# Performance work log

Measured on AMD Instinct MI355X. Metric: run time of the kernel, lower is better.

## Reference

```python
import jax, jax.numpy as jnp
import numpy as np

N_NODES, N_EDGES = 50000, 800000
IN_X, OUT_X = 32, 64
IN_EN, OUT_EN = 32, 64
HIDDEN = [64, 128, 32]  # build_mlp hidden sizes


def _mlp_params(key, dims):
    ps = []
    for i, (a, b) in enumerate(zip(dims[:-1], dims[1:])):
        k1, k2, key = jax.random.split(key, 3)
        s = 1.0 / np.sqrt(a)
        ps.append(jax.random.uniform(k1, (a, b), jnp.float32, -s, s))
        ps.append(jax.random.uniform(k2, (b,), jnp.float32, -s, s))
    return ps


def _mlp_apply(h, params):
    n_layers = len(params) // 2
    for i in range(n_layers):
        W, b = params[2 * i], params[2 * i + 1]
        h = h @ W + b
        if i < n_layers - 1:
            h = jax.nn.relu(h)
    return h


def setup_inputs() -> dict:
    key = jax.random.key(0)
    kx, ken, ks, kd, kt, kp, k_ten, k_pen = jax.random.split(key, 8)
    inp = {
        "x": jax.random.normal(kx, (N_NODES, IN_X), jnp.float32),
        "en": jax.random.normal(ken, (N_NODES, IN_EN), jnp.float32),
        "src": jax.random.randint(ks, (N_EDGES,), 0, N_NODES),
        "dst": jax.random.randint(kd, (N_EDGES,), 0, N_NODES),
    }
    # linear layers theta/phi for x
    kt1, kt2 = jax.random.split(kt)
    kp1, kp2 = jax.random.split(kp)
    s = 1.0 / np.sqrt(IN_X)
    inp["theta_W"] = jax.random.uniform(kt1, (IN_X, OUT_X), jnp.float32, -s, s)
    inp["theta_b"] = jax.random.uniform(kt2, (OUT_X,), jnp.float32, -s, s)
    inp["phi_W"] = jax.random.uniform(kp1, (IN_X, OUT_X), jnp.float32, -s, s)
    inp["phi_b"] = jax.random.uniform(kp2, (OUT_X,), jnp.float32, -s, s)
    # MLPs theta_en / phi_en: in_en -> 64 -> 128 -> 32 -> out_en
    dims = [IN_EN] + HIDDEN + [OUT_EN]
    for name, p in zip(
        ["ten_W0", "ten_b0", "ten_W1", "ten_b1", "ten_W2", "ten_b2", "ten_W3", "ten_b3"],
        _mlp_params(k_ten, dims)):
        inp[name] = p
    for name, p in zip(
        ["pen_W0", "pen_b0", "pen_W1", "pen_b1", "pen_W2", "pen_b2", "pen_W3", "pen_b3"],
        _mlp_params(k_pen, dims)):
        inp[name] = p
    return inp


def reference(x, en, src, dst,
              theta_W, theta_b, phi_W, phi_b,
              ten_W0, ten_b0, ten_W1, ten_b1, ten_W2, ten_b2, ten_W3, ten_b3,
              pen_W0, pen_b0, pen_W1, pen_b1, pen_W2, pen_b2, pen_W3, pen_b3):
    n = x.shape[0]
    ten = [ten_W0, ten_b0, ten_W1, ten_b1, ten_W2, ten_b2, ten_W3, ten_b3]
    pen = [pen_W0, pen_b0, pen_W1, pen_b1, pen_W2, pen_b2, pen_W3, pen_b3]

    # --- message: per-edge features ---
    dx = x[dst] - x[src]                       # [E, in_x]
    edge_x = dx @ theta_W + theta_b + (x @ phi_W + phi_b)[src]   # [E, out_x]
    den = en[dst] - en[src]                    # [E, in_en]
    edge_en = _mlp_apply(den, ten) + _mlp_apply(en, pen)[src]    # [E, out_en]

    # --- aggregate: max over incoming edge_x, mean over incoming edge_en ---
    deg = jax.ops.segment_sum(jnp.ones((src.shape[0],), x.dtype), dst, num_segments=n)
    has_in = (deg > 0)[:, None]
    x_new = jax.ops.segment_max(edge_x, dst, num_segments=n)
    x_new = jnp.where(has_in, x_new, 0.0)      # DGL zero-fills empty nodes
    en_sum = jax.ops.segment_sum(edge_en, dst, num_segments=n)
    en_new = en_sum / jnp.maximum(deg, 1.0)[:, None]

    # knn_graph rebuild is a library call (excluded from the kernel target);
    # return the updated node features carried by the new graph.
    return jnp.concatenate([x_new, en_new], axis=-1)  # [N, out_x + out_en]
```

## Files before the change

### kernel.cpp

```cpp
#include <hip/hip_runtime.h>

#define N_NODES 50000
#define N_EDGES 800000

typedef __attribute__((ext_vector_type(8))) short short8v;
typedef __attribute__((ext_vector_type(4))) float f32x4;

constexpr int M_W0T = 0;
constexpr int M_B0  = 2048;
constexpr int M_W1T = 2112;
constexpr int M_B1  = 10304;
constexpr int M_W2  = 10432;
constexpr int M_B2  = 14528;
constexpr int M_SZ  = 14560;

__device__ __forceinline__ void stage_mlp(float* sm,
    const float* __restrict__ W0, const float* __restrict__ b0,
    const float* __restrict__ W1, const float* __restrict__ b1,
    const float* __restrict__ W2, const float* __restrict__ b2,
    int tid, int nthr) {
  for (int t = tid; t < 2048; t += nthr) {
    int j = t >> 5, k = t & 31;
    sm[M_W0T + t] = W0[k * 64 + j];
  }
  for (int t = tid; t < 8192; t += nthr) {
    int k2 = t >> 6, j = t & 63;
    sm[M_W1T + t] = W1[j * 128 + k2];
  }
  for (int t = tid; t < 4096; t += nthr) sm[M_W2 + t] = W2[t];
  for (int t = tid; t < 64; t += nthr)  sm[M_B0 + t] = b0[t];
  for (int t = tid; t < 128; t += nthr) sm[M_B1 + t] = b1[t];
  for (int t = tid; t < 32; t += nthr)  sm[M_B2 + t] = b2[t];
}

__device__ __forceinline__ void mlp_core(const float* sm, const float den[32],
                                         float h2[32]) {
  float h0[64];
#pragma unroll
  for (int j = 0; j < 64; ++j) {
    float a = sm[M_B0 + j];
#pragma unroll
    for (int k = 0; k < 32; ++k) a += den[k] * sm[M_W0T + j * 32 + k];
    h0[j] = fmaxf(a, 0.f);
  }
#pragma unroll
  for (int j = 0; j < 32; ++j) h2[j] = sm[M_B2 + j];
  for (int k2 = 0; k2 < 128; ++k2) {
    float t = sm[M_B1 + k2];
#pragma unroll
    for (int j = 0; j < 64; ++j) t += h0[j] * sm[M_W1T + k2 * 64 + j];
    t = fmaxf(t, 0.f);
#pragma unroll
    for (int j = 0; j < 32; ++j) h2[j] += t * sm[M_W2 + k2 * 32 + j];
  }
#pragma unroll
  for (int j = 0; j < 32; ++j) h2[j] = fmaxf(h2[j], 0.f);
}

__device__ __forceinline__ ushort bf16hi(float v) {
  return (ushort)(__float_as_uint(v) >> 16);
}

constexpr int EK_TW0 = 0;
constexpr int EK_MLP = 2048;
constexpr int EK_W3T = 16608;
constexpr int EK_B3  = 18656;
constexpr int EK_SZ  = 18720;

#define CA_EN 196
#define CA_CNT 3125
#define CA_PACK 48

__global__ void __launch_bounds__(256) combo_a_kernel(
    const float* __restrict__ en, const float* __restrict__ tW0,
    const float* __restrict__ pW0, const float* __restrict__ pb0,
    const float* __restrict__ pW1, const float* __restrict__ pb1,
    const float* __restrict__ pW2, const float* __restrict__ pb2,
    const float* __restrict__ pW3, const float* __restrict__ pb3,
    float* __restrict__ gp, float* __restrict__ u,
    const int* __restrict__ dst, int* __restrict__ counts,
    const float* __restrict__ tW1, const float* __restrict__ tW2,
    ushort* __restrict__ wp) {
  const int b = blockIdx.x;
  const int tid = threadIdx.x;
  if (b < CA_EN) {
    __shared__ __align__(16) float sm[EK_SZ];
    for (int t = tid; t < 2048; t += 256) {
      int j = t >> 5, k = t & 31;
      sm[EK_TW0 + t] = tW0[k * 64 + j];
      sm[EK_W3T + t] = pW3[k * 64 + j];
    }
    for (int t = tid; t < 64; t += 256) sm[EK_B3 + t] = pb3[t];
    stage_mlp(sm + EK_MLP, pW0, pb0, pW1, pb1, pW2, pb2, tid, 256);
    __syncthreads();
    int n = b * 256 + tid;
    if (n >= N_NODES) return;

    float ev[32];
    {
      const float4* p = (const float4*)(en + (long)n * 32);
#pragma unroll
      for (int q = 0; q < 8; ++q) {
        float4 v = p[q];
        ev[q * 4 + 0] = v.x; ev[q * 4 + 1] = v.y;
        ev[q * 4 + 2] = v.z; ev[q * 4 + 3] = v.w;
      }
    }
    float* uo = u + (long)n * 64;
    for (int j = 0; j < 64; ++j) {
      float a = 0.f;
#pragma unroll
      for (int k = 0; k < 32; ++k) a += ev[k] * sm[EK_TW0 + j * 32 + k];
      uo[j] = a;
    }
    float h2p[32];
    mlp_core(sm + EK_MLP, ev, h2p);
    float* go = gp + (long)n * 128 + 64;
    for (int j = 0; j < 64; ++j) {
      float o = sm[EK_B3 + j];
#pragma unroll
      for (int k = 0; k < 32; ++k) o += h2p[k] * sm[EK_W3T + j * 32 + k];
      go[j] = o;
    }
  } else if (b < CA_EN + CA_CNT) {
    int e = (b - CA_EN) * 256 + tid;
    if (e < N_EDGES) atomicAdd(&counts[dst[e]], 1);
  } else {
    int t = (b - CA_EN - CA_CNT) * 256 + tid;
    if (t >= 12288) return;
    float v;
    int hi_off, lo_off;
    if (t < 8192) {
      int fi = t >> 9, lane = (t >> 3) & 63, j = t & 7;
      int r = fi >> 1, f = fi & 1;
      int k2 = r * 16 + (lane & 15);
      int jg = f * 32 + (lane >> 4) * 8 + j;
      v = tW1[jg * 128 + k2];
      hi_off = t; lo_off = 8192 + t;
    } else {
      int t2 = t - 8192;
      int fi = t2 >> 9, lane = (t2 >> 3) & 63, j = t2 & 7;
      int tt = fi >> 2, f2 = fi & 3;
      int cc = tt * 16 + (lane & 15);
      int q = (lane >> 4) & 3;
      int k2 = f2 * 32 + (j >> 2) * 16 + q * 4 + (j & 3);
      v = tW2[k2 * 32 + cc];
      hi_off = 16384 + t2; lo_off = 20480 + t2;
    }
    ushort h = bf16hi(v);
    float hf = __uint_as_float((unsigned)h << 16);
    ushort l = bf16hi(v - hf);
    wp[hi_off] = h;
    wp[lo_off] = l;
  }
}

#define SCAN_NB ((N_NODES + 1023) / 1024)

__global__ void __launch_bounds__(1024) scan1_kernel(
    const int* __restrict__ counts, int* __restrict__ offsets,
    int* __restrict__ bsum) {
  __shared__ int wsum[16];
  int t = threadIdx.x, b = blockIdx.x;
  int idx = b * 1024 + t;
  int c = (idx < N_NODES) ? counts[idx] : 0;
  int lane = t & 63, w = t >> 6;
  int v = c;
#pragma unroll
  for (int off = 1; off < 64; off <<= 1) {
    int tt = __shfl_up(v, off);
    if (lane >= off) v += tt;
  }
  if (lane == 63) wsum[w] = v;
  __syncthreads();
  int wpre = 0;
#pragma unroll
  for (int i = 0; i < 16; ++i) {
    int tt = wsum[i];
    if (i < w) wpre += tt;
  }
  int incl = v + wpre;
  if (idx < N_NODES) offsets[idx] = incl - c;
  if (t == 1023) bsum[b] = incl;
}

__global__ void __launch_bounds__(1024) scan2_kernel(
    const int* __restrict__ bsum, int* __restrict__ offsets,
    int* __restrict__ counts) {
  __shared__ int sb[SCAN_NB];
  int t = threadIdx.x, b = blockIdx.x;
  if (t < SCAN_NB) sb[t] = bsum[t];
  __syncthreads();
  int bpre = 0;
#pragma unroll
  for (int i = 0; i < SCAN_NB; ++i) {
    int tt = sb[i];
    if (i < b) bpre += tt;
  }
  int idx = b * 1024 + t;
  if (idx < N_NODES) {
    int v = offsets[idx] + bpre;
    offsets[idx] = v;
    counts[idx] = v;
  }
  if (b == 0 && t == 0) offsets[N_NODES] = N_EDGES;
}

#define CB_X 196
#define CB_SC 3125

constexpr int XK_THT = 0;
constexpr int XK_PHT = 2048;
constexpr int XK_THB = 4096;
constexpr int XK_PHB = 4160;
constexpr int XK_SZ  = 4224;

__global__ void __launch_bounds__(256) combo_b_kernel(
    const float* __restrict__ x,
    const float* __restrict__ thW, const float* __restrict__ thB,
    const float* __restrict__ phW, const float* __restrict__ phB,
    float* __restrict__ out, float* __restrict__ gp,
    const int* __restrict__ src, const int* __restrict__ dst,
    int* __restrict__ cursor, int2* __restrict__ csr) {
  const int b = blockIdx.x;
  const int tid = threadIdx.x;
  if (b < CB_X) {
    __shared__ __align__(16) float sm[XK_SZ];
    for (int t = tid; t < 2048; t += 256) {
      int j = t >> 5, k = t & 31;
      sm[XK_THT + t] = thW[k * 64 + j];
      sm[XK_PHT + t] = phW[k * 64 + j];
    }
    for (int t = tid; t < 64; t += 256) {
      sm[XK_THB + t] = thB[t];
      sm[XK_PHB + t] = phB[t];
    }
    __syncthreads();
    int n = b * 256 + tid;
    if (n >= N_NODES) return;

    float xv[32];
    {
      const float4* p = (const float4*)(x + (long)n * 32);
#pragma unroll
      for (int q = 0; q < 8; ++q) {
        float4 v = p[q];
        xv[q * 4 + 0] = v.x; xv[q * 4 + 1] = v.y;
        xv[q * 4 + 2] = v.z; xv[q * 4 + 3] = v.w;
      }
    }
    float* ao = out + (long)n * 128;
    float* go = gp + (long)n * 128;
    for (int j = 0; j < 64; ++j) {
      float dth = 0.f, dph = 0.f;
#pragma unroll
      for (int k = 0; k < 32; ++k) {
        dth += xv[k] * sm[XK_THT + j * 32 + k];
        dph += xv[k] * sm[XK_PHT + j * 32 + k];
      }
      ao[j] = sm[XK_THB + j] + dth;
      go[j] = sm[XK_PHB + j] + dph - dth;
    }
  } else {
    int e = (b - CB_X) * 256 + tid;
    if (e >= N_EDGES) return;
    int d = dst[e];
    int slot = atomicAdd(&cursor[d], 1);
    csr[slot] = make_int2(src[e], d);
  }
}

__global__ void __launch_bounds__(512) mlp_edge_kernel(
    const float* __restrict__ u,
    const int2* __restrict__ csr,
    const float* __restrict__ b0g, const float* __restrict__ b1g,
    const float* __restrict__ b2g,
    const ushort* __restrict__ wp,
    float* __restrict__ h2sum) {
  __shared__ __align__(16) ushort lds[24576];
  {
    const uint4* s4 = (const uint4*)wp;
    uint4* d4 = (uint4*)lds;
    for (int i = threadIdx.x; i < 3072; i += 512) d4[i] = s4[i];
  }
  __syncthreads();

  const int orig = blockIdx.x;
  const int xcd = orig & 7, loc = orig >> 3;
  const int blk = (xcd < 2) ? xcd * 782 + loc
                            : 2 * 782 + (xcd - 2) * 781 + loc;

  const int lane = threadIdx.x & 63;
  const int q = lane >> 4, c = lane & 15;
  const int wv = threadIdx.x >> 6;
  const int e = (blk * 8 + wv) * 16 + c;
  const int2 pr = csr[e];
  const int s = pr.x, d = pr.y;

  const short8v* W1HI = (const short8v*)(lds);
  const short8v* W1LO = (const short8v*)(lds + 8192);
  const short8v* W2HI = (const short8v*)(lds + 16384);
  const short8v* W2LO = (const short8v*)(lds + 20480);

  short8v bh0, bl0, bh1, bl1;
  {
    const float* ud = u + (long)d * 64 + q * 8;
    const float* us = u + (long)s * 64 + q * 8;
    const float* bp = b0g + q * 8;
#pragma unroll
    for (int f = 0; f < 2; ++f) {
      float4 d0 = *(const float4*)(ud + f * 32);
      float4 d1 = *(const float4*)(ud + f * 32 + 4);
      float4 s0 = *(const float4*)(us + f * 32);
      float4 s1 = *(const float4*)(us + f * 32 + 4);
      float4 c0 = *(const float4*)(bp + f * 32);
      float4 c1 = *(const float4*)(bp + f * 32 + 4);
      float v[8];
      v[0] = fmaxf(d0.x - s0.x + c0.x, 0.f);
      v[1] = fmaxf(d0.y - s0.y + c0.y, 0.f);
      v[2] = fmaxf(d0.z - s0.z + c0.z, 0.f);
      v[3] = fmaxf(d0.w - s0.w + c0.w, 0.f);
      v[4] = fmaxf(d1.x - s1.x + c1.x, 0.f);
      v[5] = fmaxf(d1.y - s1.y + c1.y, 0.f);
      v[6] = fmaxf(d1.z - s1.z + c1.z, 0.f);
      v[7] = fmaxf(d1.w - s1.w + c1.w, 0.f);
      short8v hh, ll;
#pragma unroll
      for (int j = 0; j < 8; ++j) {
        unsigned uv = __float_as_uint(v[j]);
        hh[j] = (short)(uv >> 16);
        float hf = __uint_as_float(uv & 0xFFFF0000u);
        ll[j] = (short)(__float_as_uint(v[j] - hf) >> 16);
      }
      if (f == 0) { bh0 = hh; bl0 = ll; } else { bh1 = hh; bl1 = ll; }
    }
  }

  f32x4 acc[8];
#pragma unroll
  for (int r = 0; r < 8; ++r)
    acc[r] = *(const f32x4*)(b1g + r * 16 + q * 4);
#pragma unroll
  for (int r = 0; r < 8; ++r) {
    short8v ah0 = W1HI[(2 * r) * 64 + lane];
    short8v ah1 = W1HI[(2 * r + 1) * 64 + lane];
    short8v al0 = W1LO[(2 * r) * 64 + lane];
    short8v al1 = W1LO[(2 * r + 1) * 64 + lane];
    acc[r] = __builtin_amdgcn_mfma_f32_16x16x32_bf16(ah0, bh0, acc[r], 0, 0, 0);
    acc[r] = __builtin_amdgcn_mfma_f32_16x16x32_bf16(ah1, bh1, acc[r], 0, 0, 0);
    acc[r] = __builtin_amdgcn_mfma_f32_16x16x32_bf16(al0, bh0, acc[r], 0, 0, 0);
    acc[r] = __builtin_amdgcn_mfma_f32_16x16x32_bf16(al1, bh1, acc[r], 0, 0, 0);
    acc[r] = __builtin_amdgcn_mfma_f32_16x16x32_bf16(ah0, bl0, acc[r], 0, 0, 0);
    acc[r] = __builtin_amdgcn_mfma_f32_16x16x32_bf16(ah1, bl1, acc[r], 0, 0, 0);
  }
  float h1v[8][4];
#pragma unroll
  for (int r = 0; r < 8; ++r)
#pragma unroll
    for (int g = 0; g < 4; ++g) h1v[r][g] = fmaxf(acc[r][g], 0.f);

  short8v b2h[4], b2l[4];
#pragma unroll
  for (int f2 = 0; f2 < 4; ++f2) {
    short8v hh, ll;
#pragma unroll
    for (int j = 0; j < 8; ++j) {
      float v = h1v[2 * f2 + (j >> 2)][j & 3];
      unsigned uv = __float_as_uint(v);
      hh[j] = (short)(uv >> 16);
      float hf = __uint_as_float(uv & 0xFFFF0000u);
      ll[j] = (short)(__float_as_uint(v - hf) >> 16);
    }
    b2h[f2] = hh; b2l[f2] = ll;
  }

  f32x4 a20 = *(const f32x4*)(b2g + q * 4);
  f32x4 a21 = *(const f32x4*)(b2g + 16 + q * 4);
#pragma unroll
  for (int f2 = 0; f2 < 4; ++f2) {
    short8v ah = W2HI[f2 * 64 + lane];
    short8v al = W2LO[f2 * 64 + lane];
    a20 = __builtin_amdgcn_mfma_f32_16x16x32_bf16(ah, b2h[f2], a20, 0, 0, 0);
    a20 = __builtin_amdgcn_mfma_f32_16x16x32_bf16(al, b2h[f2], a20, 0, 0, 0);
    a20 = __builtin_amdgcn_mfma_f32_16x16x32_bf16(ah, b2l[f2], a20, 0, 0, 0);
    short8v ah1 = W2HI[(4 + f2) * 64 + lane];
    short8v al1 = W2LO[(4 + f2) * 64 + lane];
    a21 = __builtin_amdgcn_mfma_f32_16x16x32_bf16(ah1, b2h[f2], a21, 0, 0, 0);
    a21 = __builtin_amdgcn_mfma_f32_16x16x32_bf16(al1, b2h[f2], a21, 0, 0, 0);
    a21 = __builtin_amdgcn_mfma_f32_16x16x32_bf16(ah1, b2l[f2], a21, 0, 0, 0);
  }
  float h2v[8];
#pragma unroll
  for (int g = 0; g < 4; ++g) {
    h2v[g] = fmaxf(a20[g], 0.f);
    h2v[4 + g] = fmaxf(a21[g], 0.f);
  }

  int dp = __shfl_up(d, 1, 16);
  bool head = (c == 0) || (dp != d);
  int seg = head ? c : 0;
#pragma unroll
  for (int off = 1; off < 16; off <<= 1) {
    int t = __shfl_up(seg, off, 16);
    if (c >= off) seg = max(seg, t);
  }
#pragma unroll
  for (int off = 1; off < 16; off <<= 1) {
    bool take = (c - off) >= seg;
#pragma unroll
    for (int k = 0; k < 8; ++k) {
      float t = __shfl_up(h2v[k], off, 16);
      if (take) h2v[k] += t;
    }
  }
  int dn = __shfl_down(d, 1, 16);
  bool tail = (c == 15) || (dn != d);
  if (tail) {
    float* hs = h2sum + (long)d * 32 + q * 4;
#pragma unroll
    for (int g = 0; g < 4; ++g) atomicAdd(&hs[g], h2v[g]);
#pragma unroll
    for (int g = 0; g < 4; ++g) atomicAdd(&hs[16 + g], h2v[4 + g]);
  }
}

__global__ void __launch_bounds__(256) gather_kernel(
    const int2* __restrict__ csr, const int* __restrict__ offsets,
    const float* __restrict__ gp, const float* __restrict__ h2sum,
    const float* __restrict__ tW3, const float* __restrict__ tb3,
    float* __restrict__ out) {
  __shared__ float sW3[2048 + 64];
  for (int t = threadIdx.x; t < 2048; t += 256) sW3[t] = tW3[t];
  for (int t = threadIdx.x; t < 64; t += 256) sW3[2048 + t] = tb3[t];
  __syncthreads();
  int n = blockIdx.x * 8 + (threadIdx.x >> 5);
  int l = threadIdx.x & 31;
  int half = l >> 4, j4 = l & 15;
  int off = half * 64 + j4 * 4;
  int o0 = offsets[n], o1 = offsets[n + 1];
  int deg = o1 - o0;

  const float NEG = -3.402823466e38f;
  float4 mx = make_float4(NEG, NEG, NEG, NEG);
  float4 sm4 = make_float4(0.f, 0.f, 0.f, 0.f);
  for (int t = o0; t < o1; ++t) {
    int s = csr[t].x;
    float4 v = *(const float4*)(gp + (long)s * 128 + off);
    mx.x = fmaxf(mx.x, v.x); mx.y = fmaxf(mx.y, v.y);
    mx.z = fmaxf(mx.z, v.z); mx.w = fmaxf(mx.w, v.w);
    sm4.x += v.x; sm4.y += v.y; sm4.z += v.z; sm4.w += v.w;
  }

  float4 r;
  if (half == 0) {
    float4 a = *(const float4*)(out + (long)n * 128 + off);
    bool has = deg > 0;
    r.x = has ? a.x + mx.x : 0.f;
    r.y = has ? a.y + mx.y : 0.f;
    r.z = has ? a.z + mx.z : 0.f;
    r.w = has ? a.w + mx.w : 0.f;
  } else {
    int jj = j4 * 4;
    float w30 = 0.f, w31 = 0.f, w32 = 0.f, w33 = 0.f;
    const float* h2r = h2sum + (long)n * 32;
#pragma unroll
    for (int k = 0; k < 32; ++k) {
      float h = h2r[k];
      const float* wrow = &sW3[k * 64 + jj];
      w30 += h * wrow[0]; w31 += h * wrow[1];
      w32 += h * wrow[2]; w33 += h * wrow[3];
    }
    float dg = (float)deg;
    float inv = 1.f / fmaxf(dg, 1.f);
    r.x = (sm4.x + w30 + dg * sW3[2048 + jj + 0]) * inv;
    r.y = (sm4.y + w31 + dg * sW3[2048 + jj + 1]) * inv;
    r.z = (sm4.z + w32 + dg * sW3[2048 + jj + 2]) * inv;
    r.w = (sm4.w + w33 + dg * sW3[2048 + jj + 3]) * inv;
  }
  *(float4*)(out + (long)n * 128 + off) = r;
}

extern "C" void kernel_launch(void* const* d_in, const int* in_sizes, int n_in,
                              void* d_out, int out_size, void* d_ws,
                              size_t ws_size, hipStream_t stream) {
  const float* x   = (const float*)d_in[0];
  const float* en  = (const float*)d_in[1];
  const int* src   = (const int*)d_in[2];
  const int* dst   = (const int*)d_in[3];
  const float* thW = (const float*)d_in[4];
  const float* thB = (const float*)d_in[5];
  const float* phW = (const float*)d_in[6];
  const float* phB = (const float*)d_in[7];
  const float* tW0 = (const float*)d_in[8];
  const float* tb0 = (const float*)d_in[9];
  const float* tW1 = (const float*)d_in[10];
  const float* tb1 = (const float*)d_in[11];
  const float* tW2 = (const float*)d_in[12];
  const float* tb2 = (const float*)d_in[13];
  const float* tW3 = (const float*)d_in[14];
  const float* tb3 = (const float*)d_in[15];
  const float* pW0 = (const float*)d_in[16];
  const float* pb0 = (const float*)d_in[17];
  const float* pW1 = (const float*)d_in[18];
  const float* pb1 = (const float*)d_in[19];
  const float* pW2 = (const float*)d_in[20];
  const float* pb2 = (const float*)d_in[21];
  const float* pW3 = (const float*)d_in[22];
  const float* pb3 = (const float*)d_in[23];

  float* out = (float*)d_out;
  float* ws  = (float*)d_ws;
  float* gp     = ws;
  float* u      = ws + (long)N_NODES * 128;
  float* h2sum  = ws + (long)N_NODES * 192;
  float* wpf    = ws + (long)N_NODES * 224;
  ushort* wp    = (ushort*)wpf;
  int* iw       = (int*)(wpf + 12288);
  int2* csr     = (int2*)iw;
  int* counts   = iw + 2 * N_EDGES;
  int* offsets  = counts + N_NODES;
  int* bsum     = offsets + N_NODES + 1;

  hipMemsetAsync(counts, 0, N_NODES * sizeof(int), stream);
  hipMemsetAsync(h2sum, 0, (size_t)N_NODES * 32 * sizeof(float), stream);
  combo_a_kernel<<<CA_EN + CA_CNT + CA_PACK, 256, 0, stream>>>(
      en, tW0, pW0, pb0, pW1, pb1, pW2, pb2, pW3, pb3, gp, u,
      dst, counts, tW1, tW2, wp);
  scan1_kernel<<<SCAN_NB, 1024, 0, stream>>>(counts, offsets, bsum);
  scan2_kernel<<<SCAN_NB, 1024, 0, stream>>>(bsum, offsets, counts);
  combo_b_kernel<<<CB_X + CB_SC, 256, 0, stream>>>(
      x, thW, thB, phW, phB, out, gp, src, dst, counts, csr);
  mlp_edge_kernel<<<N_EDGES / 128, 512, 0, stream>>>(
      u, csr, tb0, tb1, tb2, wp, h2sum);
  gather_kernel<<<N_NODES / 8, 256, 0, stream>>>(
      csr, offsets, gp, h2sum, tW3, tb3, out);
}
```

Baseline: 355.2 us.

## Move per-node phi_en MLP and theta_en projection onto split-bf16 MFMA

The per-node MLP (phi_en) and the node-level theta_en first-layer projection previously ran as scalar FP32 loops from LDS, one thread per node. They now run on 16x16x32 bf16 MFMA with a hi/lo split of the weights, prepacked into a shared buffer. The x-linear work moves into the first combo kernel, and the node MLP joins the CSR scatter kernel, so the MLP can consume the packed weights. This aims to cut the ALU-bound per-node MLP cost, at the price of a larger packing stage, 72KB of LDS per block, and three-product split-bf16 accuracy instead of full FP32.

```diff
diff --git a/kernel.cpp b/kernel.cpp
--- a/kernel.cpp
+++ b/kernel.cpp
@@ -6,128 +6,85 @@
 typedef __attribute__((ext_vector_type(8))) short short8v;
 typedef __attribute__((ext_vector_type(4))) float f32x4;
 
-constexpr int M_W0T = 0;
-constexpr int M_B0  = 2048;
-constexpr int M_W1T = 2112;
-constexpr int M_B1  = 10304;
-constexpr int M_W2  = 10432;
-constexpr int M_B2  = 14528;
-constexpr int M_SZ  = 14560;
-
-__device__ __forceinline__ void stage_mlp(float* sm,
-    const float* __restrict__ W0, const float* __restrict__ b0,
-    const float* __restrict__ W1, const float* __restrict__ b1,
-    const float* __restrict__ W2, const float* __restrict__ b2,
-    int tid, int nthr) {
-  for (int t = tid; t < 2048; t += nthr) {
-    int j = t >> 5, k = t & 31;
-    sm[M_W0T + t] = W0[k * 64 + j];
-  }
-  for (int t = tid; t < 8192; t += nthr) {
-    int k2 = t >> 6, j = t & 63;
-    sm[M_W1T + t] = W1[j * 128 + k2];
-  }
-  for (int t = tid; t < 4096; t += nthr) sm[M_W2 + t] = W2[t];
-  for (int t = tid; t < 64; t += nthr)  sm[M_B0 + t] = b0[t];
-  for (int t = tid; t < 128; t += nthr) sm[M_B1 + t] = b1[t];
-  for (int t = tid; t < 32; t += nthr)  sm[M_B2 + t] = b2[t];
-}
-
-__device__ __forceinline__ void mlp_core(const float* sm, const float den[32],
-                                         float h2[32]) {
-  float h0[64];
-#pragma unroll
-  for (int j = 0; j < 64; ++j) {
-    float a = sm[M_B0 + j];
-#pragma unroll
-    for (int k = 0; k < 32; ++k) a += den[k] * sm[M_W0T + j * 32 + k];
-    h0[j] = fmaxf(a, 0.f);
-  }
-#pragma unroll
-  for (int j = 0; j < 32; ++j) h2[j] = sm[M_B2 + j];
-  for (int k2 = 0; k2 < 128; ++k2) {
-    float t = sm[M_B1 + k2];
-#pragma unroll
-    for (int j = 0; j < 64; ++j) t += h0[j] * sm[M_W1T + k2 * 64 + j];
-    t = fmaxf(t, 0.f);
-#pragma unroll
-    for (int j = 0; j < 32; ++j) h2[j] += t * sm[M_W2 + k2 * 32 + j];
-  }
-#pragma unroll
-  for (int j = 0; j < 32; ++j) h2[j] = fmaxf(h2[j], 0.f);
-}
-
 __device__ __forceinline__ ushort bf16hi(float v) {
   return (ushort)(__float_as_uint(v) >> 16);
 }
 
-constexpr int EK_TW0 = 0;
-constexpr int EK_MLP = 2048;
-constexpr int EK_W3T = 16608;
-constexpr int EK_B3  = 18656;
-constexpr int EK_SZ  = 18720;
-
-#define CA_EN 196
-#define CA_CNT 3125
-#define CA_PACK 48
-
-__global__ void __launch_bounds__(256) combo_a_kernel(
-    const float* __restrict__ en, const float* __restrict__ tW0,
-    const float* __restrict__ pW0, const float* __restrict__ pb0,
-    const float* __restrict__ pW1, const float* __restrict__ pb1,
-    const float* __restrict__ pW2, const float* __restrict__ pb2,
-    const float* __restrict__ pW3, const float* __restrict__ pb3,
-    float* __restrict__ gp, float* __restrict__ u,
+__device__ __forceinline__ void split8(const float v[8], short8v& hh, short8v& ll) {
+#pragma unroll
+  for (int j = 0; j < 8; ++j) {
+    unsigned uv = __float_as_uint(v[j]);
+    hh[j] = (short)(uv >> 16);
+    float hf = __uint_as_float(uv & 0xFFFF0000u);
+    ll[j] = (short)(__float_as_uint(v[j] - hf) >> 16);
+  }
+}
+
+#define C1_X 196
+#define C1_CNT 3125
+#define C1_PACK 120
+
+constexpr int XK_THT = 0;
+constexpr int XK_PHT = 2048;
+constexpr int XK_THB = 4096;
+constexpr int XK_PHB = 4160;
+constexpr int XK_SZ  = 4224;
+
+__global__ void __launch_bounds__(256) combo1_kernel(
+    const float* __restrict__ x,
+    const float* __restrict__ thW, const float* __restrict__ thB,
+    const float* __restrict__ phW, const float* __restrict__ phB,
+    float* __restrict__ out, float* __restrict__ gp,
     const int* __restrict__ dst, int* __restrict__ counts,
     const float* __restrict__ tW1, const float* __restrict__ tW2,
-    ushort* __restrict__ wp) {
+    const float* __restrict__ tW0, const float* __restrict__ pW0,
+    const float* __restrict__ pW1, const float* __restrict__ pW2,
+    const float* __restrict__ pW3, ushort* __restrict__ wp) {
   const int b = blockIdx.x;
   const int tid = threadIdx.x;
-  if (b < CA_EN) {
-    __shared__ __align__(16) float sm[EK_SZ];
+  if (b < C1_X) {
+    __shared__ __align__(16) float sm[XK_SZ];
     for (int t = tid; t < 2048; t += 256) {
       int j = t >> 5, k = t & 31;
-      sm[EK_TW0 + t] = tW0[k * 64 + j];
-      sm[EK_W3T + t] = pW3[k * 64 + j];
-    }
-    for (int t = tid; t < 64; t += 256) sm[EK_B3 + t] = pb3[t];
-    stage_mlp(sm + EK_MLP, pW0, pb0, pW1, pb1, pW2, pb2, tid, 256);
+      sm[XK_THT + t] = thW[k * 64 + j];
+      sm[XK_PHT + t] = phW[k * 64 + j];
+    }
+    for (int t = tid; t < 64; t += 256) {
+      sm[XK_THB + t] = thB[t];
+      sm[XK_PHB + t] = phB[t];
+    }
     __syncthreads();
     int n = b * 256 + tid;
     if (n >= N_NODES) return;
 
-    float ev[32];
+    float xv[32];
     {
-      const float4* p = (const float4*)(en + (long)n * 32);
+      const float4* p = (const float4*)(x + (long)n * 32);
 #pragma unroll
       for (int q = 0; q < 8; ++q) {
         float4 v = p[q];
-        ev[q * 4 + 0] = v.x; ev[q * 4 + 1] = v.y;
-        ev[q * 4 + 2] = v.z; ev[q * 4 + 3] = v.w;
+        xv[q * 4 + 0] = v.x; xv[q * 4 + 1] = v.y;
+        xv[q * 4 + 2] = v.z; xv[q * 4 + 3] = v.w;
       }
     }
-    float* uo = u + (long)n * 64;
+    float* ao = out + (long)n * 128;
+    float* go = gp + (long)n * 128;
     for (int j = 0; j < 64; ++j) {
-      float a = 0.f;
-#pragma unroll
-      for (int k = 0; k < 32; ++k) a += ev[k] * sm[EK_TW0 + j * 32 + k];
-      uo[j] = a;
-    }
-    float h2p[32];
-    mlp_core(sm + EK_MLP, ev, h2p);
-    float* go = gp + (long)n * 128 + 64;
-    for (int j = 0; j < 64; ++j) {
-      float o = sm[EK_B3 + j];
-#pragma unroll
-      for (int k = 0; k < 32; ++k) o += h2p[k] * sm[EK_W3T + j * 32 + k];
-      go[j] = o;
-    }
-  } else if (b < CA_EN + CA_CNT) {
-    int e = (b - CA_EN) * 256 + tid;
+      float dth = 0.f, dph = 0.f;
+#pragma unroll
+      for (int k = 0; k < 32; ++k) {
+        dth += xv[k] * sm[XK_THT + j * 32 + k];
+        dph += xv[k] * sm[XK_PHT + j * 32 + k];
+      }
+      ao[j] = sm[XK_THB + j] + dth;
+      go[j] = sm[XK_PHB + j] + dph - dth;
+    }
+  } else if (b < C1_X + C1_CNT) {
+    int e = (b - C1_X) * 256 + tid;
     if (e < N_EDGES) atomicAdd(&counts[dst[e]], 1);
   } else {
-    int t = (b - CA_EN - CA_CNT) * 256 + tid;
-    if (t >= 12288) return;
+    int t = (b - C1_X - C1_CNT) * 256 + tid;
+    if (t >= 30720) return;
     float v;
     int hi_off, lo_off;
     if (t < 8192) {
@@ -137,15 +94,49 @@
       int jg = f * 32 + (lane >> 4) * 8 + j;
       v = tW1[jg * 128 + k2];
       hi_off = t; lo_off = 8192 + t;
-    } else {
+    } else if (t < 12288) {
       int t2 = t - 8192;
       int fi = t2 >> 9, lane = (t2 >> 3) & 63, j = t2 & 7;
       int tt = fi >> 2, f2 = fi & 3;
       int cc = tt * 16 + (lane & 15);
-      int q = (lane >> 4) & 3;
-      int k2 = f2 * 32 + (j >> 2) * 16 + q * 4 + (j & 3);
+      int qq = (lane >> 4) & 3;
+      int k2 = f2 * 32 + (j >> 2) * 16 + qq * 4 + (j & 3);
       v = tW2[k2 * 32 + cc];
       hi_off = 16384 + t2; lo_off = 20480 + t2;
+    } else if (t < 16384) {
+      int t3 = t - 12288;
+      const float* M = (t3 < 2048) ? tW0 : pW0;
+      int tt3 = t3 & 2047;
+      int fi = tt3 >> 9, lane = (tt3 >> 3) & 63, j = tt3 & 7;
+      int row = fi * 16 + (lane & 15);
+      int k = (lane >> 4) * 8 + j;
+      v = M[k * 64 + row];
+      hi_off = ((t3 < 2048) ? 24576 : 28672) + tt3;
+      lo_off = hi_off + 2048;
+    } else if (t < 24576) {
+      int t5 = t - 16384;
+      int fi = t5 >> 9, lane = (t5 >> 3) & 63, j = t5 & 7;
+      int r = fi >> 1, f = fi & 1;
+      int row = r * 16 + (lane & 15);
+      int sig = 32 * f + 16 * (j >> 2) + 4 * ((lane >> 4) & 3) + (j & 3);
+      v = pW1[sig * 128 + row];
+      hi_off = 32768 + t5; lo_off = 40960 + t5;
+    } else if (t < 28672) {
+      int t6 = t - 24576;
+      int fi = t6 >> 9, lane = (t6 >> 3) & 63, j = t6 & 7;
+      int tt = fi >> 2, f2 = fi & 3;
+      int cc = tt * 16 + (lane & 15);
+      int qq = (lane >> 4) & 3;
+      int k2 = f2 * 32 + (j >> 2) * 16 + qq * 4 + (j & 3);
+      v = pW2[k2 * 32 + cc];
+      hi_off = 49152 + t6; lo_off = 53248 + t6;
+    } else {
+      int t7 = t - 28672;
+      int fi = t7 >> 9, lane = (t7 >> 3) & 63, j = t7 & 7;
+      int row = fi * 16 + (lane & 15);
+      int sig = 16 * (j >> 2) + 4 * ((lane >> 4) & 3) + (j & 3);
+      v = pW3[sig * 64 + row];
+      hi_off = 57344 + t7; lo_off = 59392 + t7;
     }
     ushort h = bf16hi(v);
     float hf = __uint_as_float((unsigned)h << 16);
@@ -206,63 +197,144 @@
   if (b == 0 && t == 0) offsets[N_NODES] = N_EDGES;
 }
 
-#define CB_X 196
-#define CB_SC 3125
-
-constexpr int XK_THT = 0;
-constexpr int XK_PHT = 2048;
-constexpr int XK_THB = 4096;
-constexpr int XK_PHB = 4160;
-constexpr int XK_SZ  = 4224;
-
-__global__ void __launch_bounds__(256) combo_b_kernel(
-    const float* __restrict__ x,
-    const float* __restrict__ thW, const float* __restrict__ thB,
-    const float* __restrict__ phW, const float* __restrict__ phB,
-    float* __restrict__ out, float* __restrict__ gp,
+#define C2_EN 391
+#define C2_SC 1563
+
+__global__ void __launch_bounds__(512) combo2_kernel(
+    const float* __restrict__ en, const ushort* __restrict__ wp,
+    const float* __restrict__ pb0, const float* __restrict__ pb1,
+    const float* __restrict__ pb2, const float* __restrict__ pb3,
+    float* __restrict__ u, float* __restrict__ gp,
     const int* __restrict__ src, const int* __restrict__ dst,
     int* __restrict__ cursor, int2* __restrict__ csr) {
   const int b = blockIdx.x;
   const int tid = threadIdx.x;
-  if (b < CB_X) {
-    __shared__ __align__(16) float sm[XK_SZ];
-    for (int t = tid; t < 2048; t += 256) {
-      int j = t >> 5, k = t & 31;
-      sm[XK_THT + t] = thW[k * 64 + j];
-      sm[XK_PHT + t] = phW[k * 64 + j];
-    }
-    for (int t = tid; t < 64; t += 256) {
-      sm[XK_THB + t] = thB[t];
-      sm[XK_PHB + t] = phB[t];
+  if (b < C2_EN) {
+    __shared__ __align__(16) ushort lds[36864];
+    {
+      const uint4* s4 = (const uint4*)(wp + 24576);
+      uint4* d4 = (uint4*)lds;
+      for (int i = tid; i < 4608; i += 512) d4[i] = s4[i];
     }
     __syncthreads();
-    int n = b * 256 + tid;
-    if (n >= N_NODES) return;
-
-    float xv[32];
+    const int lane = tid & 63, q = lane >> 4, c = lane & 15, wv = tid >> 6;
+    const int n = (b * 8 + wv) * 16 + c;
+    const bool valid = n < N_NODES;
+
+    float env[8];
+#pragma unroll
+    for (int j = 0; j < 8; ++j) env[j] = 0.f;
+    if (valid) {
+      const float4* p = (const float4*)(en + (long)n * 32 + q * 8);
+      float4 e0 = p[0], e1 = p[1];
+      env[0] = e0.x; env[1] = e0.y; env[2] = e0.z; env[3] = e0.w;
+      env[4] = e1.x; env[5] = e1.y; env[6] = e1.z; env[7] = e1.w;
+    }
+    short8v beh, bel;
+    split8(env, beh, bel);
+
+    const short8v* TW0H = (const short8v*)(lds);
+    const short8v* TW0L = (const short8v*)(lds + 2048);
+    const short8v* PW0H = (const short8v*)(lds + 4096);
+    const short8v* PW0L = (const short8v*)(lds + 6144);
+    const short8v* NW1H = (const short8v*)(lds + 8192);
+    const short8v* NW1L = (const short8v*)(lds + 16384);
+    const short8v* NW2H = (const short8v*)(lds + 24576);
+    const short8v* NW2L = (const short8v*)(lds + 28672);
+    const short8v* NW3H = (const short8v*)(lds + 32768);
+    const short8v* NW3L = (const short8v*)(lds + 34816);
+
+#pragma unroll
+    for (int t = 0; t < 4; ++t) {
+      f32x4 a = {0.f, 0.f, 0.f, 0.f};
+      short8v ah = TW0H[t * 64 + lane], al = TW0L[t * 64 + lane];
+      a = __builtin_amdgcn_mfma_f32_16x16x32_bf16(ah, beh, a, 0, 0, 0);
+      a = __builtin_amdgcn_mfma_f32_16x16x32_bf16(al, beh, a, 0, 0, 0);
+      a = __builtin_amdgcn_mfma_f32_16x16x32_bf16(ah, bel, a, 0, 0, 0);
+      if (valid) *(f32x4*)(u + (long)n * 64 + t * 16 + q * 4) = a;
+    }
+
+    float h0v[4][4];
+#pragma unroll
+    for (int t = 0; t < 4; ++t) {
+      f32x4 a = *(const f32x4*)(pb0 + t * 16 + q * 4);
+      short8v ah = PW0H[t * 64 + lane], al = PW0L[t * 64 + lane];
+      a = __builtin_amdgcn_mfma_f32_16x16x32_bf16(ah, beh, a, 0, 0, 0);
+      a = __builtin_amdgcn_mfma_f32_16x16x32_bf16(al, beh, a, 0, 0, 0);
+      a = __builtin_amdgcn_mfma_f32_16x16x32_bf16(ah, bel, a, 0, 0, 0);
+#pragma unroll
+      for (int g = 0; g < 4; ++g) h0v[t][g] = fmaxf(a[g], 0.f);
+    }
+
+    short8v b1h[2], b1l[2];
+#pragma unroll
+    for (int f = 0; f < 2; ++f) {
+      float tmp[8];
+#pragma unroll
+      for (int j = 0; j < 8; ++j) tmp[j] = h0v[2 * f + (j >> 2)][j & 3];
+      split8(tmp, b1h[f], b1l[f]);
+    }
+
+    float h1v[8][4];
+#pragma unroll
+    for (int r = 0; r < 8; ++r) {
+      f32x4 a = *(const f32x4*)(pb1 + r * 16 + q * 4);
+#pragma unroll
+      for (int f = 0; f < 2; ++f) {
+        short8v ah = NW1H[(r * 2 + f) * 64 + lane];
+        short8v al = NW1L[(r * 2 + f) * 64 + lane];
+        a = __builtin_amdgcn_mfma_f32_16x16x32_bf16(ah, b1h[f], a, 0, 0, 0);
+        a = __builtin_amdgcn_mfma_f32_16x16x32_bf16(al, b1h[f], a, 0, 0, 0);
+        a = __builtin_amdgcn_mfma_f32_16x16x32_bf16(ah, b1l[f], a, 0, 0, 0);
+      }
+#pragma unroll
+      for (int g = 0; g < 4; ++g) h1v[r][g] = fmaxf(a[g], 0.f);
+    }
+
+    short8v b2h[4], b2l[4];
+#pragma unroll
+    for (int f2 = 0; f2 < 4; ++f2) {
+      float tmp[8];
+#pragma unroll
+      for (int j = 0; j < 8; ++j) tmp[j] = h1v[2 * f2 + (j >> 2)][j & 3];
+      split8(tmp, b2h[f2], b2l[f2]);
+    }
+
+    float h2v[2][4];
+#pragma unroll
+    for (int tt = 0; tt < 2; ++tt) {
+      f32x4 a = *(const f32x4*)(pb2 + tt * 16 + q * 4);
+#pragma unroll
+      for (int f2 = 0; f2 < 4; ++f2) {
+        short8v ah = NW2H[(tt * 4 + f2) * 64 + lane];
+        short8v al = NW2L[(tt * 4 + f2) * 64 + lane];
+        a = __builtin_amdgcn_mfma_f32_16x16x32_bf16(ah, b2h[f2], a, 0, 0, 0);
+        a = __builtin_amdgcn_mfma_f32_16x16x32_bf16(al, b2h[f2], a, 0, 0, 0);
+        a = __builtin_amdgcn_mfma_f32_16x16x32_bf16(ah, b2l[f2], a, 0, 0, 0);
+      }
+#pragma unroll
+      for (int g = 0; g < 4; ++g) h2v[tt][g] = fmaxf(a[g], 0.f);
+    }
+
+    short8v b3h, b3l;
     {
-      const float4* p = (const float4*)(x + (long)n * 32);
-#pragma unroll
-      for (int q = 0; q < 8; ++q) {
-        float4 v = p[q];
-        xv[q * 4 + 0] = v.x; xv[q * 4 + 1] = v.y;
-        xv[q * 4 + 2] = v.z; xv[q * 4 + 3] = v.w;
-      }
-    }
-    float* ao = out + (long)n * 128;
-    float* go = gp + (long)n * 128;
-    for (int j = 0; j < 64; ++j) {
-      float dth = 0.f, dph = 0.f;
-#pragma unroll
-      for (int k = 0; k < 32; ++k) {
-        dth += xv[k] * sm[XK_THT + j * 32 + k];
-        dph += xv[k] * sm[XK_PHT + j * 32 + k];
-      }
-      ao[j] = sm[XK_THB + j] + dth;
-      go[j] = sm[XK_PHB + j] + dph - dth;
+      float tmp[8];
+#pragma unroll
+      for (int j = 0; j < 8; ++j) tmp[j] = h2v[j >> 2][j & 3];
+      split8(tmp, b3h, b3l);
+    }
+
+#pragma unroll
+    for (int t = 0; t < 4; ++t) {
+      f32x4 a = *(const f32x4*)(pb3 + t * 16 + q * 4);
+      short8v ah = NW3H[t * 64 + lane], al = NW3L[t * 64 + lane];
+      a = __builtin_amdgcn_mfma_f32_16x16x32_bf16(ah, b3h, a, 0, 0, 0);
+      a = __builtin_amdgcn_mfma_f32_16x16x32_bf16(al, b3h, a, 0, 0, 0);
+      a = __builtin_amdgcn_mfma_f32_16x16x32_bf16(ah, b3l, a, 0, 0, 0);
+      if (valid) *(f32x4*)(gp + (long)n * 128 + 64 + t * 16 + q * 4) = a;
     }
   } else {
-    int e = (b - CB_X) * 256 + tid;
+    int e = (b - C2_EN) * 512 + tid;
     if (e >= N_EDGES) return;
     int d = dst[e];
     int slot = atomicAdd(&cursor[d], 1);
@@ -325,13 +397,7 @@
       v[6] = fmaxf(d1.z - s1.z + c1.z, 0.f);
       v[7] = fmaxf(d1.w - s1.w + c1.w, 0.f);
       short8v hh, ll;
-#pragma unroll
-      for (int j = 0; j < 8; ++j) {
-        unsigned uv = __float_as_uint(v[j]);
-        hh[j] = (short)(uv >> 16);
-        float hf = __uint_as_float(uv & 0xFFFF0000u);
-        ll[j] = (short)(__float_as_uint(v[j] - hf) >> 16);
-      }
+      split8(v, hh, ll);
       if (f == 0) { bh0 = hh; bl0 = ll; } else { bh1 = hh; bl1 = ll; }
     }
   }
@@ -362,16 +428,10 @@
   short8v b2h[4], b2l[4];
 #pragma unroll
   for (int f2 = 0; f2 < 4; ++f2) {
-    short8v hh, ll;
-#pragma unroll
-    for (int j = 0; j < 8; ++j) {
-      float v = h1v[2 * f2 + (j >> 2)][j & 3];
-      unsigned uv = __float_as_uint(v);
-      hh[j] = (short)(uv >> 16);
-      float hf = __uint_as_float(uv & 0xFFFF0000u);
-      ll[j] = (short)(__float_as_uint(v - hf) >> 16);
-    }
-    b2h[f2] = hh; b2l[f2] = ll;
+    float tmp[8];
+#pragma unroll
+    for (int j = 0; j < 8; ++j) tmp[j] = h1v[2 * f2 + (j >> 2)][j & 3];
+    split8(tmp, b2h[f2], b2l[f2]);
   }
 
   f32x4 a20 = *(const f32x4*)(b2g + q * 4);
@@ -515,7 +575,7 @@
   float* h2sum  = ws + (long)N_NODES * 192;
   float* wpf    = ws + (long)N_NODES * 224;
   ushort* wp    = (ushort*)wpf;
-  int* iw       = (int*)(wpf + 12288);
+  int* iw       = (int*)(wpf + 30720);
   int2* csr     = (int2*)iw;
   int* counts   = iw + 2 * N_EDGES;
   int* offsets  = counts + N_NODES;
@@ -523,13 +583,13 @@
 
   hipMemsetAsync(counts, 0, N_NODES * sizeof(int), stream);
   hipMemsetAsync(h2sum, 0, (size_t)N_NODES * 32 * sizeof(float), stream);
-  combo_a_kernel<<<CA_EN + CA_CNT + CA_PACK, 256, 0, stream>>>(
-      en, tW0, pW0, pb0, pW1, pb1, pW2, pb2, pW3, pb3, gp, u,
-      dst, counts, tW1, tW2, wp);
+  combo1_kernel<<<C1_X + C1_CNT + C1_PACK, 256, 0, stream>>>(
+      x, thW, thB, phW, phB, out, gp, dst, counts,
+      tW1, tW2, tW0, pW0, pW1, pW2, pW3, wp);
   scan1_kernel<<<SCAN_NB, 1024, 0, stream>>>(counts, offsets, bsum);
   scan2_kernel<<<SCAN_NB, 1024, 0, stream>>>(bsum, offsets, counts);
-  combo_b_kernel<<<CB_X + CB_SC, 256, 0, stream>>>(
-      x, thW, thB, phW, phB, out, gp, src, dst, counts, csr);
+  combo2_kernel<<<C2_EN + C2_SC, 512, 0, stream>>>(
+      en, wp, pb0, pb1, pb2, pb3, u, gp, src, dst, counts, csr);
   mlp_edge_kernel<<<N_EDGES / 128, 512, 0, stream>>>(
       u, csr, tb0, tb1, tb2, wp, h2sum);
   gather_kernel<<<N_NODES / 8, 256, 0, stream>>>(
```

New measurement: 316.7 us. -10.9%, faster.
